# Performance work log

Measured on AMD Instinct MI355X. Metric: run time of the kernel, lower is better.

Reference implementation:

```python
import jax, jax.numpy as jnp
import numpy as np
from jax import lax

N = 5000            # number of detections
FEAT = 1024         # last-layer feature dim; 1024 + 9 engineered feats = indim 1033
DIMS = [FEAT + 9, 1000, 600, 300, 150, 1]
IOU_THRESH = 0.5
EPS = 2.220446049250313e-16  # sys.float_info.epsilon


def setup_inputs() -> dict:
    key = jax.random.key(0)
    ks = jax.random.split(key, 8 + 3 * len(DIMS))
    H, W = 800.0, 1333.0
    cx = jax.random.uniform(ks[0], (N,), minval=0.0, maxval=W)
    cy = jax.random.uniform(ks[1], (N,), minval=0.0, maxval=H)
    bw = jax.random.uniform(ks[2], (N,), minval=20.0, maxval=250.0)
    bh = jax.random.uniform(ks[3], (N,), minval=20.0, maxval=250.0)
    x1 = jnp.clip(cx - bw / 2, 0.0, W - 2)
    y1 = jnp.clip(cy - bh / 2, 0.0, H - 2)
    x2 = jnp.clip(cx + bw / 2, x1 + 1, W)
    y2 = jnp.clip(cy + bh / 2, y1 + 1, H)
    inp = {
        'multi_bboxes': jnp.stack([x1, y1, x2, y2], axis=1),
        'cls_score': jax.random.uniform(ks[4], (N, 2)),
        'last_layer_feats': jax.random.normal(ks[5], (N, FEAT)),
        'img_shape': jnp.array([H, W], jnp.float32),
    }
    # PermEqui2_mean params: Gamma (weight+bias) and Lambda (weight only)
    ki = 6
    for i, (din, dout) in enumerate(zip(DIMS[:-1], DIMS[1:])):
        s = 1.0 / np.sqrt(din)
        inp[f'Wg{i+1}'] = jax.random.uniform(ks[ki], (dout, din), minval=-s, maxval=s); ki += 1
        inp[f'bg{i+1}'] = jax.random.uniform(ks[ki], (dout,), minval=-s, maxval=s); ki += 1
        inp[f'Wl{i+1}'] = jax.random.uniform(ks[ki], (dout, din), minval=-s, maxval=s); ki += 1
    return inp


def _greedy_cluster(ious, thresh):
    # Sequential greedy IoU clustering (NMS-like). assign[i] = index of cluster seed.
    n = ious.shape[0]

    def step(carry, inp):
        is_c, assign = carry
        j, row = inp
        seed = is_c[j]
        hit = row > thresh
        member = seed & hit & is_c
        assign = jnp.where(member, j, assign)
        is_c = is_c & ~(seed & hit)
        return (is_c, assign), None

    init = (jnp.ones(n, bool), jnp.zeros(n, jnp.int32))
    (_, assign), _ = lax.scan(step, init, (jnp.arange(n, dtype=jnp.int32), ious))
    return assign


def _forward(multi_bboxes, cls_score, last_layer_feats, img_shape, params):
    n = multi_bboxes.shape[0]
    scores = cls_score[:, 1]
    order = jnp.argsort(-scores)
    scores = scores[order]
    bboxes = multi_bboxes[order]
    feats = last_layer_feats[order]

    x1, y1, x2, y2 = bboxes[:, 0], bboxes[:, 1], bboxes[:, 2], bboxes[:, 3]
    # pairwise IoU with the +1 pixel convention from bbox_overlaps
    iw = jnp.clip(jnp.minimum(x2[:, None], x2[None, :]) - jnp.maximum(x1[:, None], x1[None, :]) + 1, 0)
    ih = jnp.clip(jnp.minimum(y2[:, None], y2[None, :]) - jnp.maximum(y1[:, None], y1[None, :]) + 1, 0)
    area = (x2 - x1 + 1) * (y2 - y1 + 1)
    overlap = iw * ih
    ious = overlap / (area[:, None] + area[None, :] - overlap)

    assign = _greedy_cluster(lax.stop_gradient(ious), IOU_THRESH)
    counts = jax.ops.segment_sum(jnp.ones(n, jnp.float32), assign, num_segments=n)
    cden = jnp.maximum(counts, 1.0)

    Himg, Wimg = img_shape[0], img_shape[1]
    # source double-normalizes: width = (x2/W - x1/W)/W, height = (y2/H - y1/H)/H
    width = (x2 / Wimg - x1 / Wimg) / Wimg
    height = (y2 / Himg - y1 / Himg) / Himg
    areaf = width * height
    ar = width / (height + EPS)
    x = jnp.concatenate([
        bboxes, feats,
        width[:, None], height[:, None], ar[:, None], areaf[:, None], scores[:, None],
    ], axis=1)  # [n, 1033]

    def perm_equi(x, Wg, bg, Wl):
        # xm = per-set mean; x*Gamma^T + b - (xm*Lambda^T), gathered back per box
        xm = jax.ops.segment_sum(x, assign, num_segments=n) / cden[:, None]
        return x @ Wg.T + bg - (xm @ Wl.T)[assign]

    for i in range(5):
        x = jax.nn.elu(perm_equi(x, params[f'Wg{i+1}'], params[f'bg{i+1}'], params[f'Wl{i+1}']))

    # source skips singleton sets (nonzero().squeeze() -> 0-dim): mask them out
    valid = counts[assign] >= 2.0
    return jnp.where(valid[:, None], x, 0.0)  # [n, 1] per-box set logits


def reference(multi_bboxes, cls_score, last_layer_feats, img_shape,
              Wg1, bg1, Wl1, Wg2, bg2, Wl2, Wg3, bg3, Wl3,
              Wg4, bg4, Wl4, Wg5, bg5, Wl5):
    params = {'Wg1': Wg1, 'bg1': bg1, 'Wl1': Wl1, 'Wg2': Wg2, 'bg2': bg2, 'Wl2': Wl2,
              'Wg3': Wg3, 'bg3': bg3, 'Wl3': Wl3, 'Wg4': Wg4, 'bg4': bg4, 'Wl4': Wl4,
              'Wg5': Wg5, 'bg5': bg5, 'Wl5': Wl5}
    return _forward(multi_bboxes, cls_score, last_layer_feats, img_shape, params)
```

## Files before the change

### kernel.cpp

```cpp
#include <hip/hip_runtime.h>
#include <cstdint>
#include <cstddef>

#define N_BOX 5000
#define NW    80
#define LDX   1040
#define LDZ   2048
#define LDYM  1000
#define LDW   1040
#define LDAB  2080
#define NCHUNK ((N_BOX + 63) / 64)
#define RT    ((N_BOX + 255) / 256)

typedef short bf16x8 __attribute__((ext_vector_type(8)));
typedef float f32x4v __attribute__((ext_vector_type(4)));
typedef unsigned short u16x8 __attribute__((ext_vector_type(8)));

__device__ __forceinline__ float fence_f(float x) { asm volatile("" : "+v"(x)); return x; }

__device__ __forceinline__ unsigned short f2bf(float x) {
    unsigned u = __builtin_bit_cast(unsigned, x);
    unsigned r = (u + 0x7FFFu + ((u >> 16) & 1u)) >> 16;
    return (unsigned short)r;
}
__device__ __forceinline__ float bf2f(unsigned short h) {
    unsigned u = ((unsigned)h) << 16;
    return __builtin_bit_cast(float, u);
}

__global__ void rank_partial_kernel(const float* __restrict__ cls, int* __restrict__ rank) {
    __shared__ float sj[256];
    int t = threadIdx.x;
    int jbase = blockIdx.y * 256;
    int jg = jbase + t;
    sj[t] = (jg < N_BOX) ? cls[2 * jg + 1] : 0.0f;
    __syncthreads();
    int i = blockIdx.x * 256 + t;
    if (i >= N_BOX) return;
    float si = cls[2 * i + 1];
    int jmax = (N_BOX - jbase < 256) ? (N_BOX - jbase) : 256;
    int r = 0;
    for (int k = 0; k < jmax; ++k) {
        float sjv = sj[k];
        int j = jbase + k;
        r += (sjv > si) || (sjv == si && j < i);
    }
    atomicAdd(&rank[i], r);
}

__global__ void rank_scatter_kernel(const int* __restrict__ rank, int* __restrict__ ord) {
    int i = blockIdx.x * blockDim.x + threadIdx.x;
    if (i < N_BOX) ord[rank[i]] = i;
}

__global__ void gather_kernel(const float* __restrict__ bb, const float* __restrict__ cls,
                              const float* __restrict__ feats, const float* __restrict__ img,
                              const int* __restrict__ ord,
                              float* __restrict__ X0, float* __restrict__ sb) {
    int r = blockIdx.x;
    int i = ord[r];
    float x1 = bb[4 * i + 0], y1 = bb[4 * i + 1], x2 = bb[4 * i + 2], y2 = bb[4 * i + 3];
    float H = img[0], W = img[1];
    float sc = cls[2 * i + 1];
    if (threadIdx.x == 0) {
        sb[0 * N_BOX + r] = x1;
        sb[1 * N_BOX + r] = y1;
        sb[2 * N_BOX + r] = x2;
        sb[3 * N_BOX + r] = y2;
        sb[4 * N_BOX + r] = (x2 - x1 + 1.0f) * (y2 - y1 + 1.0f);
        sb[5 * N_BOX + r] = sc;
    }
    float width  = (x2 / W - x1 / W) / W;
    float height = (y2 / H - y1 / H) / H;
    float ar     = width / (height + 2.220446049250313e-16f);
    float areaf  = width * height;
    float* row = X0 + (size_t)r * LDX;
    for (int o = threadIdx.x; o < LDX; o += blockDim.x) {
        float v;
        if (o < 4)          v = (o == 0) ? x1 : (o == 1) ? y1 : (o == 2) ? x2 : y2;
        else if (o < 1028)  v = feats[(size_t)i * 1024 + (o - 4)];
        else if (o == 1028) v = width;
        else if (o == 1029) v = height;
        else if (o == 1030) v = ar;
        else if (o == 1031) v = areaf;
        else if (o == 1032) v = sc;
        else                v = 0.0f;
        row[o] = v;
    }
}

__global__ void mask_kernel(const float* __restrict__ sb, unsigned long long* __restrict__ mask,
                            unsigned long long* __restrict__ diag, int* __restrict__ counts) {
    int j = blockIdx.x;
    if (threadIdx.x == 0) counts[j] = 0;
    const float* X1 = sb;
    const float* Y1 = sb + N_BOX;
    const float* X2 = sb + 2 * N_BOX;
    const float* Y2 = sb + 3 * N_BOX;
    const float* AR = sb + 4 * N_BOX;
    float xj1 = X1[j], yj1 = Y1[j], xj2 = X2[j], yj2 = Y2[j], aj = AR[j];
    int lane = threadIdx.x & 63;
    int wave = threadIdx.x >> 6;
    int nwav = blockDim.x >> 6;
    int dw = j >> 6;
    for (int w = wave; w < NW; w += nwav) {
        int i = w * 64 + lane;
        bool pred = false;
        if (i < N_BOX) {
            float iw = fmaxf(fminf(xj2, X2[i]) - fmaxf(xj1, X1[i]) + 1.0f, 0.0f);
            float ih = fmaxf(fminf(yj2, Y2[i]) - fmaxf(yj1, Y1[i]) + 1.0f, 0.0f);
            float ov = fence_f(iw * ih);
            float denom = fence_f((aj + AR[i]) - ov);
            pred = (ov / denom) > 0.5f;
        }
        unsigned long long b = __ballot(pred);
        if (lane == 0) {
            mask[(size_t)j * NW + w] = b;
            if (w == dw) diag[j] = b;
        }
    }
}

__device__ __forceinline__ void nms_body(const unsigned long long* __restrict__ mask,
                                         const unsigned long long* __restrict__ diag,
                                         unsigned long long* __restrict__ keep,
                                         unsigned long long* supp,
                                         unsigned long long* keep_sh,
                                         unsigned long long* rem_sh,
                                         unsigned long long* kb_sh) {
    int tid = threadIdx.x;
    int l = tid & 63;
    int w = tid >> 6;
    if (tid < 80) supp[tid] = 0ULL;
    unsigned long long dg = 0ULL, dg_next = 0ULL;
    if (w == 0) dg = diag[l];
    __syncthreads();
    for (int c = 0; c < NCHUNK; ++c) {
        if (w == 0) {
            unsigned long long curv = supp[c];
            unsigned clo = __builtin_amdgcn_readfirstlane((unsigned)curv);
            unsigned chi = __builtin_amdgcn_readfirstlane((unsigned)(curv >> 32));
            unsigned long long cur = ((unsigned long long)chi << 32) | clo;
            int jmax = (N_BOX - c * 64 < 64) ? (N_BOX - c * 64) : 64;
            unsigned long long valid = (jmax >= 64) ? ~0ULL : ((1ULL << jmax) - 1ULL);
            unsigned long long rem = ~cur & valid;
            if (l == 0) *rem_sh = rem;
        }
        __syncthreads();
        unsigned long long rem0 = *rem_sh;
        unsigned long long a0 = 0, a1 = 0, a2 = 0, a3 = 0, a4 = 0;
        unsigned long long b0 = 0, b1 = 0, b2 = 0, b3 = 0, b4 = 0;
        unsigned mym = 0;
        int base = (w - 1) * 5;
        if (w > 0) {
            mym = (base < 64) ? (unsigned)((rem0 >> base) & 31ULL) : 0u;
            const unsigned long long* rowp = mask + (size_t)(c * 64 + base) * NW;
            if (mym & 1u)  { a0 = rowp[0 * NW + l]; b0 = (l < 16) ? rowp[0 * NW + 64 + l] : 0ULL; }
            if (mym & 2u)  { a1 = rowp[1 * NW + l]; b1 = (l < 16) ? rowp[1 * NW + 64 + l] : 0ULL; }
            if (mym & 4u)  { a2 = rowp[2 * NW + l]; b2 = (l < 16) ? rowp[2 * NW + 64 + l] : 0ULL; }
            if (mym & 8u)  { a3 = rowp[3 * NW + l]; b3 = (l < 16) ? rowp[3 * NW + 64 + l] : 0ULL; }
            if (mym & 16u) { a4 = rowp[4 * NW + l]; b4 = (l < 16) ? rowp[4 * NW + 64 + l] : 0ULL; }
        } else {
            if (c + 1 < NCHUNK) dg_next = diag[(size_t)(c + 1) * 64 + l];
            unsigned rlo = __builtin_amdgcn_readfirstlane((unsigned)rem0);
            unsigned rhi = __builtin_amdgcn_readfirstlane((unsigned)(rem0 >> 32));
            unsigned long long remS = ((unsigned long long)rhi << 32) | rlo;
            unsigned long long kb = 0ULL;
            while (remS) {
                int jj = __builtin_ctzll(remS);
                kb |= 1ULL << jj;
                unsigned dlo = __builtin_amdgcn_readlane((unsigned)dg, jj);
                unsigned dhi = __builtin_amdgcn_readlane((unsigned)(dg >> 32), jj);
                unsigned long long dj = ((unsigned long long)dhi << 32) | dlo;
                remS &= ~dj;
                remS &= ~(1ULL << jj);
            }
            if (l == 0) { *kb_sh = kb; keep_sh[c] = kb; }
        }
        __syncthreads();
        if (w > 0 && mym) {
            unsigned long long kb = *kb_sh;
            unsigned kw = ((unsigned)((kb >> base) & 31ULL)) & mym;
            if (kw & 1u)  { atomicOr(&supp[l], a0); if (l < 16) atomicOr(&supp[64 + l], b0); }
            if (kw & 2u)  { atomicOr(&supp[l], a1); if (l < 16) atomicOr(&supp[64 + l], b1); }
            if (kw & 4u)  { atomicOr(&supp[l], a2); if (l < 16) atomicOr(&supp[64 + l], b2); }
            if (kw & 8u)  { atomicOr(&supp[l], a3); if (l < 16) atomicOr(&supp[64 + l], b3); }
            if (kw & 16u) { atomicOr(&supp[l], a4); if (l < 16) atomicOr(&supp[64 + l], b4); }
        }
        if (w == 0) dg = dg_next;
        __syncthreads();
    }
    if (tid < NCHUNK) keep[tid] = keep_sh[tid];
}

__global__ __launch_bounds__(1024) void nms_scan_kernel(const unsigned long long* __restrict__ mask,
                                                        const unsigned long long* __restrict__ diag,
                                                        unsigned long long* __restrict__ keep) {
    __shared__ unsigned long long supp[80];
    __shared__ unsigned long long keep_sh[NCHUNK];
    __shared__ unsigned long long rem_sh;
    __shared__ unsigned long long kb_sh;
    nms_body(mask, diag, keep, supp, keep_sh, &rem_sh, &kb_sh);
}

__device__ __forceinline__ void wconv_row(const float* __restrict__ Wg, const float* __restrict__ Wl,
                                          unsigned short* __restrict__ B2, int n, int tid2,
                                          int dout, int din, int K16) {
    unsigned short* dst = B2 + (size_t)n * LDAB;
    int K2 = 2 * K16;
    if (n >= 2 * dout) {
        for (int k = tid2; k < K2; k += 256) dst[k] = 0;
        return;
    }
    const float* src = (n < dout) ? (Wg + (size_t)n * din) : (Wl + (size_t)(n - dout) * din);
    for (int k = tid2; k < K2; k += 256) {
        int ks = (k >= K16) ? (k - K16) : k;
        float x = (ks < din) ? src[ks] : 0.0f;
        dst[k] = f2bf(x);
    }
}

__global__ __launch_bounds__(1024) void nms_gemm_fused(const unsigned long long* __restrict__ mask,
                                                       const unsigned long long* __restrict__ diag,
                                                       unsigned long long* __restrict__ keep,
                                                       const unsigned short* __restrict__ A2,
                                                       const unsigned short* __restrict__ B2,
                                                       float* __restrict__ C, int KT, int Nn,
                                                       int MTiles,
                                                       const float* __restrict__ X0,
                                                       float* __restrict__ E9, float* __restrict__ W9,
                                                       const float* __restrict__ Wg1, const float* __restrict__ Wl1,
                                                       const float* __restrict__ Wg0full, const float* __restrict__ Wl0full,
                                                       unsigned short* __restrict__ B2_1,
                                                       const float* __restrict__ Wg2, const float* __restrict__ Wl2,
                                                       unsigned short* __restrict__ B2_2,
                                                       const float* __restrict__ Wg3, const float* __restrict__ Wl3,
                                                       unsigned short* __restrict__ B2_3) {
    __shared__ __align__(16) unsigned short AsBuf[2 * 8192];
    __shared__ __align__(16) unsigned short BsBuf[2 * 8192];
    int tid = threadIdx.x;
    int b = blockIdx.x;
    if (b == 0) {
        unsigned long long* supp    = (unsigned long long*)AsBuf;
        unsigned long long* keep_sh = supp + 80;
        unsigned long long* rem_sh  = keep_sh + NCHUNK;
        unsigned long long* kb_sh   = rem_sh + 1;
        nms_body(mask, diag, keep, supp, keep_sh, rem_sh, kb_sh);
        return;
    }
    int NG = MTiles * 8;
    if (b <= NG) {
        int t = b - 1;
        size_t bm = (size_t)(t % MTiles) * 256;
        size_t bn = (size_t)(t / MTiles) * 256;
        int lane = tid & 63;
        int wavef = tid >> 6;
        int wr = wavef >> 2, wc = wavef & 3;

        f32x4v acc[4][4];
#pragma unroll
        for (int i = 0; i < 4; ++i)
#pragma unroll
            for (int j = 0; j < 4; ++j) acc[i][j] = (f32x4v){0.f, 0.f, 0.f, 0.f};

        const unsigned short* gA = A2 + (bm + wavef * 16 + (lane & 15)) * (size_t)LDAB + (lane >> 4) * 8;
        const unsigned short* gB = B2 + (bn + wavef * 16 + (lane & 15)) * (size_t)LDAB + (lane >> 4) * 8;
        unsigned ldsoff = (unsigned)((wavef * 64 + lane) * 16);

#define FSTAGE(T, BUF)                                                                             \
        {                                                                                          \
            size_t ko = (size_t)(T) * 32;                                                          \
            __builtin_amdgcn_global_load_lds(                                                      \
                (const __attribute__((address_space(1))) void*)(gA + ko),                          \
                (__attribute__((address_space(3))) void*)((char*)AsBuf + (BUF) * 16384 + ldsoff),  \
                16, 0, 0);                                                                         \
            __builtin_amdgcn_global_load_lds(                                                      \
                (const __attribute__((address_space(1))) void*)(gB + ko),                          \
                (__attribute__((address_space(3))) void*)((char*)BsBuf + (BUF) * 16384 + ldsoff),  \
                16, 0, 0);                                                                         \
        }

        FSTAGE(0, 0);
        for (int kt = 0; kt < KT; ++kt) {
            int cur = kt & 1;
            if (kt + 1 < KT) {
                FSTAGE(kt + 1, cur ^ 1);
                asm volatile("s_waitcnt vmcnt(2)" ::: "memory");
            } else {
                asm volatile("s_waitcnt vmcnt(0)" ::: "memory");
            }
            asm volatile("s_barrier" ::: "memory");
            bf16x8 af[4], bf[4];
#pragma unroll
            for (int f4 = 0; f4 < 4; ++f4) {
                af[f4] = *(const bf16x8*)((const char*)AsBuf + cur * 16384 + ((wr * 4 + f4) * 64 + lane) * 16);
                bf[f4] = *(const bf16x8*)((const char*)BsBuf + cur * 16384 + ((wc * 4 + f4) * 64 + lane) * 16);
            }
#pragma unroll
            for (int i = 0; i < 4; ++i)
#pragma unroll
                for (int j = 0; j < 4; ++j)
                    acc[i][j] = __builtin_amdgcn_mfma_f32_16x16x32_bf16(af[i], bf[j], acc[i][j], 0, 0, 0);
            asm volatile("s_barrier" ::: "memory");
        }
#undef FSTAGE

#pragma unroll
        for (int i = 0; i < 4; ++i) {
            int r0 = (int)bm + wr * 64 + i * 16 + (lane >> 4) * 4;
#pragma unroll
            for (int j = 0; j < 4; ++j) {
                int col = (int)bn + wc * 64 + j * 16 + (lane & 15);
                if (col < Nn) {
#pragma unroll
                    for (int e = 0; e < 4; ++e) {
                        int r = r0 + e;
                        if (r < N_BOX) C[(size_t)r * LDZ + col] = acc[i][j][e];
                    }
                }
            }
        }
        return;
    }
    int rb = b - 1 - NG;
    const int cq[9] = {0, 1, 2, 3, 1028, 1029, 1030, 1031, 1032};
    if (rb < 5) {
        int r = rb * 1024 + tid;
        if (r < 5120) {
            float* dst = E9 + (size_t)r * 12;
#pragma unroll
            for (int q = 0; q < 9; ++q) dst[q] = (r < N_BOX) ? X0[(size_t)r * LDX + cq[q]] : 0.0f;
            dst[9] = dst[10] = dst[11] = 0.0f;
        }
        return;
    }
    rb -= 5;
    if (rb < 2) {
        int n = rb * 1024 + tid;
        if (n < 2048) {
            float* dst = W9 + (size_t)n * 12;
            const float* src = (n < 1000) ? (Wg0full + (size_t)n * 1033)
                             : (n < 2000) ? (Wl0full + (size_t)(n - 1000) * 1033) : nullptr;
#pragma unroll
            for (int q = 0; q < 9; ++q) dst[q] = src ? src[cq[q]] : 0.0f;
            dst[9] = dst[10] = dst[11] = 0.0f;
        }
        return;
    }
    rb -= 2;
    int rowl = tid >> 8;
    int tid2 = tid & 255;
    if (rb < 320) {
        int n = rb * 4 + rowl;
        if (n < 1280) wconv_row(Wg1, Wl1, B2_1, n, tid2, 600, 1000, 1008);
        return;
    }
    rb -= 320;
    if (rb < 160) {
        int n = rb * 4 + rowl;
        if (n < 640) wconv_row(Wg2, Wl2, B2_2, n, tid2, 300, 600, 608);
        return;
    }
    rb -= 160;
    {
        int n = rb * 4 + rowl;
        if (n < 384) wconv_row(Wg3, Wl3, B2_3, n, tid2, 150, 300, 304);
        return;
    }
}

__global__ void z9_assign_kernel(float* __restrict__ Z, const float* __restrict__ E9,
                                 const float* __restrict__ W9, int Nn,
                                 const unsigned long long* __restrict__ mask,
                                 const unsigned long long* __restrict__ keep,
                                 int* __restrict__ assign, int* __restrict__ counts) {
    int b = blockIdx.x;
    if (b < N_BOX) {
        int r = b;
        float e[9];
#pragma unroll
        for (int q = 0; q < 9; ++q) e[q] = E9[(size_t)r * 12 + q];
        for (int o = threadIdx.x; o < Nn; o += blockDim.x) {
            const float* w = W9 + (size_t)o * 12;
            float s = 0.0f;
#pragma unroll
            for (int q = 0; q < 9; ++q) s += e[q] * w[q];
            Z[(size_t)r * LDZ + o] += s;
        }
        return;
    }
    int i = (b - N_BOX) * 256 + threadIdx.x;
    if (i >= N_BOX) return;
    for (int w = 0; w < NCHUNK; ++w) {
        unsigned long long m = mask[(size_t)i * NW + w] & keep[w];
        if (m) {
            int j = w * 64 + __builtin_ctzll(m);
            assign[i] = j;
            atomicAdd(&counts[j], 1);
            return;
        }
    }
}

__global__ void assign_kernel(const unsigned long long* __restrict__ mask,
                              const unsigned long long* __restrict__ keep,
                              int* __restrict__ assign, int* __restrict__ counts) {
    int i = blockIdx.x * blockDim.x + threadIdx.x;
    if (i >= N_BOX) return;
    for (int w = 0; w < NCHUNK; ++w) {
        unsigned long long m = mask[(size_t)i * NW + w] & keep[w];
        if (m) {
            int j = w * 64 + __builtin_ctzll(m);
            assign[i] = j;
            atomicAdd(&counts[j], 1);
            return;
        }
    }
}

__global__ __launch_bounds__(1024) void scan_kernel(const int* __restrict__ counts, int* __restrict__ offs) {
    __shared__ int part[1024];
    int t = threadIdx.x;
    int base = t * 5;
    int c[5];
    int s = 0;
#pragma unroll
    for (int k = 0; k < 5; ++k) {
        int idx = base + k;
        c[k] = (idx < N_BOX) ? counts[idx] : 0;
        s += c[k];
    }
    part[t] = s;
    __syncthreads();
    for (int d = 1; d < 1024; d <<= 1) {
        int v = part[t];
        int u = (t >= d) ? part[t - d] : 0;
        __syncthreads();
        part[t] = v + u;
        __syncthreads();
    }
    int run = (t > 0) ? part[t - 1] : 0;
#pragma unroll
    for (int k = 0; k < 5; ++k) {
        int idx = base + k;
        if (idx < N_BOX) offs[idx] = run;
        run += c[k];
    }
}

__global__ void rankscatter_kernel(const int* __restrict__ assign, const int* __restrict__ offs,
                                   int* __restrict__ members) {
    __shared__ int a[N_BOX];
    int tid = threadIdx.x;
    for (int t = tid; t < N_BOX; t += blockDim.x) a[t] = assign[t];
    __syncthreads();
    int i = blockIdx.x * blockDim.x + tid;
    if (i >= N_BOX) return;
    int ai = a[i];
    int r = 0;
    for (int k = 0; k < i; ++k) r += (a[k] == ai);
    members[offs[ai] + r] = i;
}

__global__ void xconv_kernel(const float* __restrict__ X, unsigned short* __restrict__ A2,
                             int K16eff, int colOff) {
    int r = blockIdx.x;
    unsigned short* dst = A2 + (size_t)r * LDAB;
    int K2 = 2 * K16eff;
    int nk8 = K2 >> 3;
    if (r >= N_BOX) {
        for (int k8 = threadIdx.x; k8 < nk8; k8 += blockDim.x) {
            u16x8 z;
#pragma unroll
            for (int j = 0; j < 8; ++j) z[j] = 0;
            *(u16x8*)(dst + (k8 << 3)) = z;
        }
        return;
    }
    const float* src = X + (size_t)r * LDX + colOff;
    for (int k8 = threadIdx.x; k8 < nk8; k8 += blockDim.x) {
        int kb = k8 << 3;
        bool lo = (kb >= K16eff);
        int ks = lo ? (kb - K16eff) : kb;
        u16x8 out;
#pragma unroll
        for (int j = 0; j < 8; ++j) {
            float x = src[ks + j];
            unsigned short ah = f2bf(x);
            out[j] = lo ? f2bf(x - bf2f(ah)) : ah;
        }
        *(u16x8*)(dst + kb) = out;
    }
}

__global__ void wconv_kernel(const float* __restrict__ Wg, const float* __restrict__ Wl,
                             unsigned short* __restrict__ B2, int dout, int din_src,
                             int din_eff, int colOff, int K16eff) {
    int n = blockIdx.x;
    unsigned short* dst = B2 + (size_t)n * LDAB;
    int K2 = 2 * K16eff;
    if (n >= 2 * dout) {
        for (int k = threadIdx.x; k < K2; k += blockDim.x) dst[k] = 0;
        return;
    }
    const float* src = (n < dout) ? (Wg + (size_t)n * din_src) : (Wl + (size_t)(n - dout) * din_src);
    for (int k = threadIdx.x; k < K2; k += blockDim.x) {
        int ks = (k >= K16eff) ? (k - K16eff) : k;
        float x = (ks < din_eff) ? src[colOff + ks] : 0.0f;
        dst[k] = f2bf(x);
    }
}

__global__ __launch_bounds__(256, 4) void gemm_mfma(const unsigned short* __restrict__ A2,
                                                    const unsigned short* __restrict__ B2,
                                                    float* __restrict__ C, int KT, int Nn) {
    __shared__ unsigned short AsBuf[2 * 4096];
    __shared__ unsigned short BsBuf[2 * 4096];
    int tid = threadIdx.x;
    int lane = tid & 63;
    int wave = tid >> 6;
    int wr = wave >> 1, wc = wave & 1;
    size_t bm = (size_t)blockIdx.x * 128;
    size_t bn = (size_t)blockIdx.y * 128;

    f32x4v acc[4][4];
#pragma unroll
    for (int i = 0; i < 4; ++i)
#pragma unroll
        for (int j = 0; j < 4; ++j) acc[i][j] = (f32x4v){0.f, 0.f, 0.f, 0.f};

    const unsigned short* gA[2];
    const unsigned short* gB[2];
    unsigned ldsoff[2];
#pragma unroll
    for (int q = 0; q < 2; ++q) {
        int f = q * 4 + wave;
        int grow = f * 16 + (lane & 15);
        int gcol = (lane >> 4) * 8;
        gA[q] = A2 + (bm + grow) * (size_t)LDAB + gcol;
        gB[q] = B2 + (bn + grow) * (size_t)LDAB + gcol;
        ldsoff[q] = (unsigned)((f * 64 + lane) * 16);
    }

#define STAGE(T, BUF)                                                                              \
    {                                                                                              \
        size_t ko = (size_t)(T) * 32;                                                              \
        _Pragma("unroll") for (int q = 0; q < 2; ++q) {                                            \
            __builtin_amdgcn_global_load_lds(                                                      \
                (const __attribute__((address_space(1))) void*)(gA[q] + ko),                       \
                (__attribute__((address_space(3))) void*)((char*)AsBuf + (BUF) * 8192 + ldsoff[q]),\
                16, 0, 0);                                                                         \
            __builtin_amdgcn_global_load_lds(                                                      \
                (const __attribute__((address_space(1))) void*)(gB[q] + ko),                       \
                (__attribute__((address_space(3))) void*)((char*)BsBuf + (BUF) * 8192 + ldsoff[q]),\
                16, 0, 0);                                                                         \
        }                                                                                          \
    }

    STAGE(0, 0);
    for (int kt = 0; kt < KT; ++kt) {
        int cur = kt & 1;
        if (kt + 1 < KT) {
            STAGE(kt + 1, cur ^ 1);
            asm volatile("s_waitcnt vmcnt(4)" ::: "memory");
        } else {
            asm volatile("s_waitcnt vmcnt(0)" ::: "memory");
        }
        asm volatile("s_barrier" ::: "memory");
        bf16x8 af[4], bf[4];
#pragma unroll
        for (int f4 = 0; f4 < 4; ++f4) {
            af[f4] = *(const bf16x8*)((const char*)AsBuf + cur * 8192 + ((wr * 4 + f4) * 64 + lane) * 16);
            bf[f4] = *(const bf16x8*)((const char*)BsBuf + cur * 8192 + ((wc * 4 + f4) * 64 + lane) * 16);
        }
#pragma unroll
        for (int i = 0; i < 4; ++i)
#pragma unroll
            for (int j = 0; j < 4; ++j)
                acc[i][j] = __builtin_amdgcn_mfma_f32_16x16x32_bf16(af[i], bf[j], acc[i][j], 0, 0, 0);
        asm volatile("s_barrier" ::: "memory");
    }
#undef STAGE

#pragma unroll
    for (int i = 0; i < 4; ++i) {
        int r0 = (int)bm + wr * 64 + i * 16 + (lane >> 4) * 4;
#pragma unroll
        for (int j = 0; j < 4; ++j) {
            int col = (int)bn + wc * 64 + j * 16 + (lane & 15);
            if (col < Nn) {
#pragma unroll
                for (int e = 0; e < 4; ++e) {
                    int r = r0 + e;
                    if (r < N_BOX) C[(size_t)r * LDZ + col] = acc[i][j][e];
                }
            }
        }
    }
}

__global__ void wcat_kernel(const float* __restrict__ Wg, const float* __restrict__ Wl,
                            float* __restrict__ Wc, int dout, int din, int K16) {
    int row = blockIdx.x;
    const float* src = (row < dout) ? (Wg + (size_t)row * din) : (Wl + (size_t)(row - dout) * din);
    float* dst = Wc + (size_t)row * LDW;
    for (int k = threadIdx.x; k < K16; k += blockDim.x)
        dst[k] = (k < din) ? src[k] : 0.0f;
}

__global__ __launch_bounds__(256) void gemm_nt(const float* __restrict__ A, const float* __restrict__ B,
                                               float* __restrict__ C, int M, int Nn, int K16) {
    __shared__ float As[16][64];
    __shared__ float Bs[16][64];
    int bm = blockIdx.x * 64;
    int bn = blockIdx.y * 64;
    int tid = threadIdx.x;
    int row = tid & 63;
    int kq  = tid >> 6;
    int tx  = tid & 15;
    int ty  = tid >> 4;
    float acc[4][4] = {};
    for (int k0 = 0; k0 < K16; k0 += 16) {
        float4 av = make_float4(0.f, 0.f, 0.f, 0.f);
        float4 bv = make_float4(0.f, 0.f, 0.f, 0.f);
        if (bm + row < M)  av = *(const float4*)&A[(size_t)(bm + row) * LDX + k0 + kq * 4];
        if (bn + row < Nn) bv = *(const float4*)&B[(size_t)(bn + row) * LDW + k0 + kq * 4];
        __syncthreads();
        As[kq * 4 + 0][row] = av.x; As[kq * 4 + 1][row] = av.y;
        As[kq * 4 + 2][row] = av.z; As[kq * 4 + 3][row] = av.w;
        Bs[kq * 4 + 0][row] = bv.x; Bs[kq * 4 + 1][row] = bv.y;
        Bs[kq * 4 + 2][row] = bv.z; Bs[kq * 4 + 3][row] = bv.w;
        __syncthreads();
#pragma unroll
        for (int kk = 0; kk < 16; ++kk) {
            float4 a = *(const float4*)&As[kk][ty * 4];
            float4 b = *(const float4*)&Bs[kk][tx * 4];
            float aa[4] = {a.x, a.y, a.z, a.w};
            float bb[4] = {b.x, b.y, b.z, b.w};
#pragma unroll
            for (int i = 0; i < 4; ++i)
#pragma unroll
                for (int jx = 0; jx < 4; ++jx) acc[i][jx] += aa[i] * bb[jx];
        }
    }
#pragma unroll
    for (int i = 0; i < 4; ++i) {
        int r = bm + ty * 4 + i;
        if (r >= M) break;
#pragma unroll
        for (int jx = 0; jx < 4; ++jx) {
            int ccol = bn + tx * 4 + jx;
            if (ccol < Nn) C[(size_t)r * LDZ + ccol] = acc[i][jx];
        }
    }
}

__global__ void segmean_kernel(const float* __restrict__ Z, int dout,
                               const int* __restrict__ counts, const int* __restrict__ offs,
                               const int* __restrict__ members, float* __restrict__ ym) {
    int j = blockIdx.x;
    int cnt = counts[j];
    if (cnt == 0) return;
    int off = offs[j];
    float fc = (float)cnt;
    for (int o = threadIdx.x; o < dout; o += blockDim.x) {
        float s = 0.0f;
        for (int m = 0; m < cnt; ++m) {
            int i = members[off + m];
            s += Z[(size_t)i * LDZ + dout + o];
        }
        ym[(size_t)j * LDYM + o] = s / fc;
    }
}

__global__ void combine_kernel(const float* __restrict__ Z, const float* __restrict__ bg,
                               const float* __restrict__ ym, const int* __restrict__ assign,
                               float* __restrict__ Xout, int dout, int doutPad) {
    int r = blockIdx.x;
    int a = assign[r];
    float* dst = Xout + (size_t)r * LDX;
    for (int o = threadIdx.x; o < doutPad; o += blockDim.x) {
        float v = 0.0f;
        if (o < dout) {
            float z = Z[(size_t)r * LDZ + o] + bg[o] - ym[(size_t)a * LDYM + o];
            v = (z > 0.0f) ? z : expm1f(z);
        }
        dst[o] = v;
    }
}

__global__ void combine_fused_kernel(const float* __restrict__ Z, const float* __restrict__ bg,
                                     const float* __restrict__ ym, const int* __restrict__ assign,
                                     unsigned short* __restrict__ A2, int dout, int K16next) {
    int r = blockIdx.x;
    int a = assign[r];
    unsigned short* dst = A2 + (size_t)r * LDAB;
    for (int o = threadIdx.x; o < K16next; o += blockDim.x) {
        float v = 0.0f;
        if (o < dout) {
            float z = Z[(size_t)r * LDZ + o] + bg[o] - ym[(size_t)a * LDYM + o];
            v = (z > 0.0f) ? z : expm1f(z);
        }
        unsigned short hi = f2bf(v);
        dst[o] = hi;
        dst[K16next + o] = f2bf(v - bf2f(hi));
    }
}

__global__ void final_kernel(const float* __restrict__ X, const int* __restrict__ assign,
                             const int* __restrict__ counts, float* __restrict__ out) {
    int r = blockIdx.x * blockDim.x + threadIdx.x;
    if (r >= N_BOX) return;
    out[r] = (counts[assign[r]] >= 2) ? X[(size_t)r * LDX] : 0.0f;
}

extern "C" void kernel_launch(void* const* d_in, const int* in_sizes, int n_in,
                              void* d_out, int out_size, void* d_ws, size_t ws_size,
                              hipStream_t stream) {
    const float* bb    = (const float*)d_in[0];
    const float* cls   = (const float*)d_in[1];
    const float* feats = (const float*)d_in[2];
    const float* img   = (const float*)d_in[3];

    char* ws = (char*)d_ws;
    size_t off = 0;
    auto alloc = [&](size_t bytes) -> void* {
        void* p = ws + off;
        off += (bytes + 255) & ~(size_t)255;
        return p;
    };
    int*   ord     = (int*)alloc((size_t)N_BOX * 4);
    int*   rankb   = (int*)alloc((size_t)N_BOX * 4);
    float* sb      = (float*)alloc((size_t)6 * N_BOX * 4);
    int*   assign  = (int*)alloc((size_t)N_BOX * 4);
    int*   counts  = (int*)alloc((size_t)N_BOX * 4);
    int*   offsb   = (int*)alloc((size_t)N_BOX * 4);
    int*   members = (int*)alloc((size_t)N_BOX * 4);
    unsigned long long* mask = (unsigned long long*)alloc((size_t)(NCHUNK * 64) * NW * 8);
    unsigned long long* diag = (unsigned long long*)alloc((size_t)NCHUNK * 64 * 8);
    unsigned long long* keep = (unsigned long long*)alloc((size_t)NCHUNK * 8 + 1024);
    float* Xa = (float*)alloc((size_t)N_BOX * LDX * 4);
    float* Xb = (float*)alloc((size_t)N_BOX * LDX * 4);
    float* Z  = (float*)alloc((size_t)N_BOX * LDZ * 4);
    float* ym = (float*)alloc((size_t)N_BOX * LDYM * 4);
    float* Wc = (float*)alloc((size_t)2000 * LDW * 4);
    unsigned short* A2   = (unsigned short*)alloc((size_t)5120 * LDAB * 2);
    unsigned short* B2_0 = (unsigned short*)alloc((size_t)2048 * LDAB * 2);
    unsigned short* B2_1 = (unsigned short*)alloc((size_t)1280 * LDAB * 2);
    unsigned short* B2_2 = (unsigned short*)alloc((size_t)640 * LDAB * 2);
    unsigned short* B2_3 = (unsigned short*)alloc((size_t)384 * LDAB * 2);
    float* E9 = (float*)alloc((size_t)5120 * 12 * 4);
    float* W9 = (float*)alloc((size_t)2048 * 12 * 4);
    bool use_mfma = (off <= ws_size);

    hipMemsetAsync(rankb, 0, (size_t)N_BOX * 4, stream);
    rank_partial_kernel<<<dim3(RT, RT), dim3(256), 0, stream>>>(cls, rankb);
    rank_scatter_kernel<<<dim3(RT), dim3(256), 0, stream>>>(rankb, ord);
    gather_kernel<<<dim3(N_BOX), dim3(256), 0, stream>>>(bb, cls, feats, img, ord, Xa, sb);
    mask_kernel<<<dim3(N_BOX), dim3(256), 0, stream>>>(sb, mask, diag, counts);

    const int dins[5]  = {1033, 1000, 600, 300, 150};
    const int douts[5] = {1000, 600, 300, 150, 1};
    const int K16e[4]  = {1024, 1008, 608, 304};
    const int coff[4]  = {4, 0, 0, 0};
    const int dineff[4] = {1024, 1000, 600, 300};
    unsigned short* B2L[4] = {B2_0, B2_1, B2_2, B2_3};

    if (use_mfma) {
        xconv_kernel<<<dim3(5120), dim3(256), 0, stream>>>(Xa, A2, K16e[0], coff[0]);
        wconv_kernel<<<dim3(2048), dim3(256), 0, stream>>>((const float*)d_in[4], (const float*)d_in[6],
                                                           B2_0, douts[0], dins[0], dineff[0], coff[0], K16e[0]);
        int KT0 = K16e[0] / 16;
        nms_gemm_fused<<<dim3(744), dim3(1024), 0, stream>>>(
            mask, diag, keep, A2, B2_0, Z, KT0, 2 * douts[0], 20,
            Xa, E9, W9,
            (const float*)d_in[7], (const float*)d_in[9],
            (const float*)d_in[4], (const float*)d_in[6],
            B2_1,
            (const float*)d_in[10], (const float*)d_in[12], B2_2,
            (const float*)d_in[13], (const float*)d_in[15], B2_3);
        z9_assign_kernel<<<dim3(N_BOX + RT), dim3(256), 0, stream>>>(Z, E9, W9, 2 * douts[0],
                                                                     mask, keep, assign, counts);
    } else {
        nms_scan_kernel<<<dim3(1), dim3(1024), 0, stream>>>(mask, diag, keep);
        assign_kernel<<<dim3(RT), dim3(256), 0, stream>>>(mask, keep, assign, counts);
    }

    scan_kernel<<<dim3(1), dim3(1024), 0, stream>>>(counts, offsb);
    rankscatter_kernel<<<dim3(RT), dim3(256), 0, stream>>>(assign, offsb, members);

    for (int L = 0; L < 5; ++L) {
        const float* Wg = (const float*)d_in[4 + 3 * L];
        const float* bg = (const float*)d_in[5 + 3 * L];
        const float* Wl = (const float*)d_in[6 + 3 * L];
        int din = dins[L], dout = douts[L];
        int K16 = (din + 15) & ~15;
        int N2 = 2 * dout;
        int doutPad = (dout + 15) & ~15;
        float* Xin  = (L % 2 == 0) ? Xa : Xb;
        float* Xout = (L % 2 == 0) ? Xb : Xa;
        if (use_mfma && L < 4) {
            if (L > 0) {
                int KT = K16e[L] / 16;
                int Ntiles = (N2 + 127) >> 7;
                gemm_mfma<<<dim3(40, Ntiles), dim3(256), 0, stream>>>(A2, B2L[L], Z, KT, N2);
            }
        } else {
            wcat_kernel<<<dim3(N2), dim3(256), 0, stream>>>(Wg, Wl, Wc, dout, din, K16);
            gemm_nt<<<dim3((N_BOX + 63) / 64, (N2 + 63) / 64), dim3(256), 0, stream>>>(Xin, Wc, Z, N_BOX, N2, K16);
        }
        segmean_kernel<<<dim3(N_BOX), dim3(256), 0, stream>>>(Z, dout, counts, offsb, members, ym);
        if (use_mfma && L < 3) {
            combine_fused_kernel<<<dim3(N_BOX), dim3(256), 0, stream>>>(Z, bg, ym, assign, A2,
                                                                        dout, K16e[L + 1]);
        } else {
            combine_kernel<<<dim3(N_BOX), dim3(256), 0, stream>>>(Z, bg, ym, assign, Xout, dout, doutPad);
        }
    }
    final_kernel<<<dim3(RT), dim3(256), 0, stream>>>(Xb, assign, counts, (float*)d_out);
}
```

Baseline: 549.5 us.

## Drop bf16 hi/lo split for later layers and specialize final layer

Later-layer activations and weights were stored as a bf16 hi+lo pair, which doubled the K dimension of those MFMA GEMMs. They are now stored as a single bf16 value, roughly halving K for layers 2-4, and the K padding is adjusted to 1024 and 320. The last layer has a single output and is replaced by three small kernels: a per-row dot product, a per-cluster mean and a combine step. This removes a padded GEMM plus segmean/combine and the final kernel. The trade is lower numerical precision from dropping the bf16 low part. An asm barrier is also added in the NMS body to force the mask loads to issue early.

```diff
diff --git a/kernel.cpp b/kernel.cpp
--- a/kernel.cpp
+++ b/kernel.cpp
@@ -160,6 +160,8 @@
             if (mym & 4u)  { a2 = rowp[2 * NW + l]; b2 = (l < 16) ? rowp[2 * NW + 64 + l] : 0ULL; }
             if (mym & 8u)  { a3 = rowp[3 * NW + l]; b3 = (l < 16) ? rowp[3 * NW + 64 + l] : 0ULL; }
             if (mym & 16u) { a4 = rowp[4 * NW + l]; b4 = (l < 16) ? rowp[4 * NW + 64 + l] : 0ULL; }
+            asm volatile("" : "+v"(a0), "+v"(a1), "+v"(a2), "+v"(a3), "+v"(a4),
+                             "+v"(b0), "+v"(b1), "+v"(b2), "+v"(b3), "+v"(b4));
         } else {
             if (c + 1 < NCHUNK) dg_next = diag[(size_t)(c + 1) * 64 + l];
             unsigned rlo = __builtin_amdgcn_readfirstlane((unsigned)rem0);
@@ -207,15 +209,13 @@
                                           unsigned short* __restrict__ B2, int n, int tid2,
                                           int dout, int din, int K16) {
     unsigned short* dst = B2 + (size_t)n * LDAB;
-    int K2 = 2 * K16;
     if (n >= 2 * dout) {
-        for (int k = tid2; k < K2; k += 256) dst[k] = 0;
+        for (int k = tid2; k < K16; k += 256) dst[k] = 0;
         return;
     }
     const float* src = (n < dout) ? (Wg + (size_t)n * din) : (Wl + (size_t)(n - dout) * din);
-    for (int k = tid2; k < K2; k += 256) {
-        int ks = (k >= K16) ? (k - K16) : k;
-        float x = (ks < din) ? src[ks] : 0.0f;
+    for (int k = tid2; k < K16; k += 256) {
+        float x = (k < din) ? src[k] : 0.0f;
         dst[k] = f2bf(x);
     }
 }
@@ -352,7 +352,7 @@
     int tid2 = tid & 255;
     if (rb < 320) {
         int n = rb * 4 + rowl;
-        if (n < 1280) wconv_row(Wg1, Wl1, B2_1, n, tid2, 600, 1000, 1008);
+        if (n < 1280) wconv_row(Wg1, Wl1, B2_1, n, tid2, 600, 1000, 1024);
         return;
     }
     rb -= 320;
@@ -364,7 +364,7 @@
     rb -= 160;
     {
         int n = rb * 4 + rowl;
-        if (n < 384) wconv_row(Wg3, Wl3, B2_3, n, tid2, 150, 300, 304);
+        if (n < 384) wconv_row(Wg3, Wl3, B2_3, n, tid2, 150, 300, 320);
         return;
     }
 }
@@ -701,10 +701,52 @@
             float z = Z[(size_t)r * LDZ + o] + bg[o] - ym[(size_t)a * LDYM + o];
             v = (z > 0.0f) ? z : expm1f(z);
         }
-        unsigned short hi = f2bf(v);
-        dst[o] = hi;
-        dst[K16next + o] = f2bf(v - bf2f(hi));
-    }
+        dst[o] = f2bf(v);
+    }
+}
+
+__global__ void l4a_kernel(const float* __restrict__ X, const float* __restrict__ Wg,
+                           const float* __restrict__ Wl, float* __restrict__ zg,
+                           float* __restrict__ zl) {
+    int r = blockIdx.x * blockDim.x + threadIdx.x;
+    if (r >= N_BOX) return;
+    const float* row = X + (size_t)r * LDX;
+    float sg = 0.0f, sl = 0.0f;
+    for (int k = 0; k < 150; ++k) {
+        float x = row[k];
+        sg += x * Wg[k];
+        sl += x * Wl[k];
+    }
+    zg[r] = sg;
+    zl[r] = sl;
+}
+
+__global__ __launch_bounds__(64) void l4b_kernel(const float* __restrict__ zl,
+                                                 const int* __restrict__ counts,
+                                                 const int* __restrict__ offs,
+                                                 const int* __restrict__ members,
+                                                 float* __restrict__ ym4) {
+    int j = blockIdx.x;
+    int cnt = counts[j];
+    if (cnt == 0) return;
+    int off = offs[j];
+    int l = threadIdx.x;
+    float s = 0.0f;
+    for (int m = l; m < cnt; m += 64) s += zl[members[off + m]];
+#pragma unroll
+    for (int d = 1; d < 64; d <<= 1) s += __shfl_xor(s, d);
+    if (l == 0) ym4[j] = s / (float)cnt;
+}
+
+__global__ void l4c_kernel(const float* __restrict__ zg, const float* __restrict__ ym4,
+                           const float* __restrict__ bg, const int* __restrict__ assign,
+                           const int* __restrict__ counts, float* __restrict__ out) {
+    int r = blockIdx.x * blockDim.x + threadIdx.x;
+    if (r >= N_BOX) return;
+    int a = assign[r];
+    float z = zg[r] + bg[0] - ym4[a];
+    float v = (z > 0.0f) ? z : expm1f(z);
+    out[r] = (counts[a] >= 2) ? v : 0.0f;
 }
 
 __global__ void final_kernel(const float* __restrict__ X, const int* __restrict__ assign,
@@ -751,6 +793,9 @@
     unsigned short* B2_3 = (unsigned short*)alloc((size_t)384 * LDAB * 2);
     float* E9 = (float*)alloc((size_t)5120 * 12 * 4);
     float* W9 = (float*)alloc((size_t)2048 * 12 * 4);
+    float* zg  = (float*)alloc((size_t)N_BOX * 4);
+    float* zl  = (float*)alloc((size_t)N_BOX * 4);
+    float* ym4 = (float*)alloc((size_t)N_BOX * 4);
     bool use_mfma = (off <= ws_size);
 
     hipMemsetAsync(rankb, 0, (size_t)N_BOX * 4, stream);
@@ -761,25 +806,23 @@
 
     const int dins[5]  = {1033, 1000, 600, 300, 150};
     const int douts[5] = {1000, 600, 300, 150, 1};
-    const int K16e[4]  = {1024, 1008, 608, 304};
-    const int coff[4]  = {4, 0, 0, 0};
-    const int dineff[4] = {1024, 1000, 600, 300};
+    const int K16s[4]  = {1024, 1024, 608, 320};
+    const int KTs[4]   = {64, 32, 19, 10};
     unsigned short* B2L[4] = {B2_0, B2_1, B2_2, B2_3};
 
     if (use_mfma) {
-        xconv_kernel<<<dim3(5120), dim3(256), 0, stream>>>(Xa, A2, K16e[0], coff[0]);
+        xconv_kernel<<<dim3(5120), dim3(256), 0, stream>>>(Xa, A2, 1024, 4);
         wconv_kernel<<<dim3(2048), dim3(256), 0, stream>>>((const float*)d_in[4], (const float*)d_in[6],
-                                                           B2_0, douts[0], dins[0], dineff[0], coff[0], K16e[0]);
-        int KT0 = K16e[0] / 16;
+                                                           B2_0, 1000, 1033, 1024, 4, 1024);
         nms_gemm_fused<<<dim3(744), dim3(1024), 0, stream>>>(
-            mask, diag, keep, A2, B2_0, Z, KT0, 2 * douts[0], 20,
+            mask, diag, keep, A2, B2_0, Z, KTs[0], 2000, 20,
             Xa, E9, W9,
             (const float*)d_in[7], (const float*)d_in[9],
             (const float*)d_in[4], (const float*)d_in[6],
             B2_1,
             (const float*)d_in[10], (const float*)d_in[12], B2_2,
             (const float*)d_in[13], (const float*)d_in[15], B2_3);
-        z9_assign_kernel<<<dim3(N_BOX + RT), dim3(256), 0, stream>>>(Z, E9, W9, 2 * douts[0],
+        z9_assign_kernel<<<dim3(N_BOX + RT), dim3(256), 0, stream>>>(Z, E9, W9, 2000,
                                                                      mask, keep, assign, counts);
     } else {
         nms_scan_kernel<<<dim3(1), dim3(1024), 0, stream>>>(mask, diag, keep);
@@ -789,33 +832,44 @@
     scan_kernel<<<dim3(1), dim3(1024), 0, stream>>>(counts, offsb);
     rankscatter_kernel<<<dim3(RT), dim3(256), 0, stream>>>(assign, offsb, members);
 
-    for (int L = 0; L < 5; ++L) {
-        const float* Wg = (const float*)d_in[4 + 3 * L];
-        const float* bg = (const float*)d_in[5 + 3 * L];
-        const float* Wl = (const float*)d_in[6 + 3 * L];
-        int din = dins[L], dout = douts[L];
-        int K16 = (din + 15) & ~15;
-        int N2 = 2 * dout;
-        int doutPad = (dout + 15) & ~15;
-        float* Xin  = (L % 2 == 0) ? Xa : Xb;
-        float* Xout = (L % 2 == 0) ? Xb : Xa;
-        if (use_mfma && L < 4) {
+    if (use_mfma) {
+        for (int L = 0; L < 4; ++L) {
+            const float* bg = (const float*)d_in[5 + 3 * L];
+            int dout = douts[L];
+            int N2 = 2 * dout;
             if (L > 0) {
-                int KT = K16e[L] / 16;
                 int Ntiles = (N2 + 127) >> 7;
-                gemm_mfma<<<dim3(40, Ntiles), dim3(256), 0, stream>>>(A2, B2L[L], Z, KT, N2);
+                gemm_mfma<<<dim3(40, Ntiles), dim3(256), 0, stream>>>(A2, B2L[L], Z, KTs[L], N2);
             }
-        } else {
+            segmean_kernel<<<dim3(N_BOX), dim3(256), 0, stream>>>(Z, dout, counts, offsb, members, ym);
+            if (L < 3) {
+                combine_fused_kernel<<<dim3(N_BOX), dim3(256), 0, stream>>>(Z, bg, ym, assign, A2,
+                                                                            dout, K16s[L + 1]);
+            } else {
+                combine_kernel<<<dim3(N_BOX), dim3(256), 0, stream>>>(Z, bg, ym, assign, Xa, dout, 160);
+            }
+        }
+        l4a_kernel<<<dim3(RT), dim3(256), 0, stream>>>(Xa, (const float*)d_in[16],
+                                                       (const float*)d_in[18], zg, zl);
+        l4b_kernel<<<dim3(N_BOX), dim3(64), 0, stream>>>(zl, counts, offsb, members, ym4);
+        l4c_kernel<<<dim3(RT), dim3(256), 0, stream>>>(zg, ym4, (const float*)d_in[17],
+                                                       assign, counts, (float*)d_out);
+    } else {
+        for (int L = 0; L < 5; ++L) {
+            const float* Wg = (const float*)d_in[4 + 3 * L];
+            const float* bg = (const float*)d_in[5 + 3 * L];
+            const float* Wl = (const float*)d_in[6 + 3 * L];
+            int din = dins[L], dout = douts[L];
+            int K16 = (din + 15) & ~15;
+            int N2 = 2 * dout;
+            int doutPad = (dout + 15) & ~15;
+            float* Xin  = (L % 2 == 0) ? Xa : Xb;
+            float* Xout = (L % 2 == 0) ? Xb : Xa;
             wcat_kernel<<<dim3(N2), dim3(256), 0, stream>>>(Wg, Wl, Wc, dout, din, K16);
             gemm_nt<<<dim3((N_BOX + 63) / 64, (N2 + 63) / 64), dim3(256), 0, stream>>>(Xin, Wc, Z, N_BOX, N2, K16);
-        }
-        segmean_kernel<<<dim3(N_BOX), dim3(256), 0, stream>>>(Z, dout, counts, offsb, members, ym);
-        if (use_mfma && L < 3) {
-            combine_fused_kernel<<<dim3(N_BOX), dim3(256), 0, stream>>>(Z, bg, ym, assign, A2,
-                                                                        dout, K16e[L + 1]);
-        } else {
+            segmean_kernel<<<dim3(N_BOX), dim3(256), 0, stream>>>(Z, dout, counts, offsb, members, ym);
             combine_kernel<<<dim3(N_BOX), dim3(256), 0, stream>>>(Z, bg, ym, assign, Xout, dout, doutPad);
         }
-    }
-    final_kernel<<<dim3(RT), dim3(256), 0, stream>>>(Xb, assign, counts, (float*)d_out);
-}
+        final_kernel<<<dim3(RT), dim3(256), 0, stream>>>(Xb, assign, counts, (float*)d_out);
+    }
+}
```

New measurement: 489.9 us. 10.9% less time.
